# Kernel tuning notes

Measured on AMD Instinct MI355X. Metric: run time of the kernel, lower is better.

The kernel has to match this reference:

```python
import jax, jax.numpy as jnp
import numpy as np

DIM = 2048
Q_C = 1536
KV_C = 512
H = 16
DH = 128
DR = 64
EPS = 1e-6
B = 4
T = 2048


def rmsnorm(x, g, eps=EPS):
    var = jnp.mean(x * x, axis=-1, keepdims=True)
    return x * jax.lax.rsqrt(var + eps) * g


def apply_rope(x, freqs_cis):
    # x: [B, t, h, d]; freqs_cis: [t, d//2, 2] (cos, sin)
    xs = x.reshape(*x.shape[:-1], -1, 2)
    x1, x2 = xs[..., 0], xs[..., 1]
    cos = freqs_cis[None, :, None, :, 0]
    sin = freqs_cis[None, :, None, :, 1]
    o1 = x1 * cos - x2 * sin
    o2 = x1 * sin + x2 * cos
    return jnp.stack([o1, o2], axis=-1).reshape(x.shape)


def setup_inputs() -> dict:
    key = jax.random.key(0)
    ks = jax.random.split(key, 12)
    s = lambda fan_in: 1.0 / np.sqrt(fan_in)
    inp = {}
    inp["x"] = jax.random.normal(ks[0], (B, T, DIM), dtype=jnp.float32)
    inp["start_pos"] = 0
    # rotary frequencies for decoupled dim
    inv_freq = 1.0 / (10000.0 ** (np.arange(0, DR, 2, dtype=np.float32) / DR))
    angles = np.arange(T, dtype=np.float32)[:, None] * inv_freq[None, :]  # [T, DR//2]
    inp["freqs_cis"] = jnp.asarray(np.stack([np.cos(angles), np.sin(angles)], axis=-1))
    # causal additive mask
    neg = jnp.float32(-1e9)
    inp["mask"] = jnp.where(jnp.tril(jnp.ones((T, T), dtype=bool)), 0.0, neg).astype(jnp.float32)
    # weights stored as (in, out)
    inp["W_dq"] = jax.random.normal(ks[1], (DIM, Q_C), dtype=jnp.float32) * s(DIM)
    inp["W_uq"] = jax.random.normal(ks[2], (Q_C, H * DH), dtype=jnp.float32) * s(Q_C)
    inp["W_dkv"] = jax.random.normal(ks[3], (DIM, KV_C), dtype=jnp.float32) * s(DIM)
    inp["W_uk"] = jax.random.normal(ks[4], (KV_C, H * DH), dtype=jnp.float32) * s(KV_C)
    inp["W_uv"] = jax.random.normal(ks[5], (KV_C, H * DH), dtype=jnp.float32) * s(KV_C)
    inp["W_qr"] = jax.random.normal(ks[6], (Q_C, H * DR), dtype=jnp.float32) * s(Q_C)
    inp["W_kr"] = jax.random.normal(ks[7], (DIM, DR), dtype=jnp.float32) * s(DIM)
    inp["W_o"] = jax.random.normal(ks[8], (H * DH, DIM), dtype=jnp.float32) * s(H * DH)
    inp["g_q"] = jnp.ones((Q_C,), dtype=jnp.float32)
    inp["g_kv"] = jnp.ones((KV_C,), dtype=jnp.float32)
    return inp


def reference(x, start_pos, freqs_cis, mask, W_dq, W_uq, W_dkv, W_uk, W_uv, W_qr, W_kr, W_o, g_q, g_kv):
    Bc, t, _ = x.shape
    q_c = rmsnorm(x @ W_dq, g_q)            # [B, t, Q_C]
    kv_c = rmsnorm(x @ W_dkv, g_kv)         # [B, t, KV_C]
    q_rope = (q_c @ W_qr).reshape(Bc, t, H, DR)
    q_rope = apply_rope(q_rope, freqs_cis)
    k_rope = apply_rope((x @ W_kr)[:, :, None, :], freqs_cis)  # [B, t, 1, DR]
    k_rope = jnp.broadcast_to(k_rope, (Bc, t, H, DR))
    q = (q_c @ W_uq).reshape(Bc, t, H, DH)
    k = (kv_c @ W_uk).reshape(Bc, t, H, DH)
    v = (kv_c @ W_uv).reshape(Bc, t, H, DH)
    q = jnp.concatenate([q, q_rope], axis=-1)  # [B, t, H, DH+DR]
    k = jnp.concatenate([k, k_rope], axis=-1)
    scale = 1.0 / np.sqrt(DH + DR)
    scores = jnp.einsum("bqhd,bkhd->bhqk", q, k) * scale + mask
    probs = jax.nn.softmax(scores, axis=-1)
    out = jnp.einsum("bhqk,bkhd->bqhd", probs, v).reshape(Bc, t, H * DH)
    return out @ W_o
```

## Files before the change

### kernel.cpp

```cpp
#include <hip/hip_runtime.h>
#include <hip/hip_bf16.h>
#include <cstdint>
#include <cstddef>

typedef unsigned short u16;
typedef __attribute__((ext_vector_type(8))) short s8v;
typedef __attribute__((ext_vector_type(4))) float f4v;

__device__ __forceinline__ float bf2f(u16 u) {
  union { unsigned u; float f; } v; v.u = ((unsigned)u) << 16; return v.f;
}
__device__ __forceinline__ u16 f2bf(float f) {
  __hip_bfloat16 h = __float2bfloat16(f);
  return *reinterpret_cast<u16*>(&h);
}

__device__ __forceinline__ void async16(u16* lds, const u16* g) {
  __builtin_amdgcn_global_load_lds((const __attribute__((address_space(1))) void*)g,
                                   (__attribute__((address_space(3))) void*)lds,
                                   16, 0, 0);
}

__global__ __launch_bounds__(256) void k_f32_to_bf16(const float* __restrict__ in,
                                                     u16* __restrict__ out, int n8) {
  int i = blockIdx.x * 256 + threadIdx.x;
  if (i >= n8) return;
  const float4* p = (const float4*)(in + (size_t)i * 8);
  float4 a = p[0], b = p[1];
  s8v ov;
  ov[0] = (short)f2bf(a.x); ov[1] = (short)f2bf(a.y);
  ov[2] = (short)f2bf(a.z); ov[3] = (short)f2bf(a.w);
  ov[4] = (short)f2bf(b.x); ov[5] = (short)f2bf(b.y);
  ov[6] = (short)f2bf(b.z); ov[7] = (short)f2bf(b.w);
  *(s8v*)(out + (size_t)i * 8) = ov;
}

__global__ __launch_bounds__(256) void k_transpose_bf16(const float* __restrict__ W,
                                                        u16* __restrict__ Wt, int K, int N) {
  __shared__ float tile[32][33];
  int n0 = blockIdx.x * 32, k0 = blockIdx.y * 32;
  int tx = threadIdx.x & 31, ty = threadIdx.x >> 5;
#pragma unroll
  for (int i = 0; i < 32; i += 8)
    tile[ty + i][tx] = W[(size_t)(k0 + ty + i) * N + n0 + tx];
  __syncthreads();
#pragma unroll
  for (int i = 0; i < 32; i += 8)
    Wt[(size_t)(n0 + ty + i) * K + k0 + tx] = f2bf(tile[tx][ty + i]);
}

template <int BM, int BN, int WVM, int WVN, int EPI>
__global__ __launch_bounds__(256, 2) void k_gemm(const u16* __restrict__ A,
                                                 const u16* __restrict__ Bt,
                                                 void* __restrict__ C0v,
                                                 void* __restrict__ C1v,
                                                 int M, int N, int K, int split) {
  constexpr int FM = BM / WVM / 16, FN = BN / WVN / 16;
  __shared__ __align__(16) u16 As[BM * 32];
  __shared__ __align__(16) u16 Bs[BN * 32];
  const int tid = threadIdx.x, wv = tid >> 6, ln = tid & 63;
  const int lo = ln & 15, hi = ln >> 4;
  const int wr = wv / WVN, wc = wv % WVN;

  int nwg = gridDim.x, bid = blockIdx.x;
  int s = (bid & 7) * (nwg >> 3) + (bid >> 3);
  int gm = M / BM;
  int m0 = (s % gm) * BM, n0 = (s / gm) * BN;

  f4v acc[FM][FN] = {};

  for (int k0 = 0; k0 < K; k0 += 32) {
    __syncthreads();
#pragma unroll
    for (int i = 0; i < BM / 64; i++) {
      int r = i * 64 + wv * 16 + (ln >> 2);
      async16(&As[(i * 64 + wv * 16) * 32],
              A + (size_t)(m0 + r) * K + k0 + (ln & 3) * 8);
    }
#pragma unroll
    for (int i = 0; i < BN / 64; i++) {
      int r = i * 64 + wv * 16 + (ln >> 2);
      async16(&Bs[(i * 64 + wv * 16) * 32],
              Bt + (size_t)(n0 + r) * K + k0 + (ln & 3) * 8);
    }
    __syncthreads();

    s8v af[FM], bf[FN];
#pragma unroll
    for (int m = 0; m < FM; m++)
      af[m] = *(const s8v*)&As[(wr * FM * 16 + m * 16 + lo) * 32 + hi * 8];
#pragma unroll
    for (int n = 0; n < FN; n++)
      bf[n] = *(const s8v*)&Bs[(wc * FN * 16 + n * 16 + lo) * 32 + hi * 8];
#pragma unroll
    for (int m = 0; m < FM; m++)
#pragma unroll
      for (int n = 0; n < FN; n++)
        acc[m][n] = __builtin_amdgcn_mfma_f32_16x16x32_bf16(af[m], bf[n], acc[m][n], 0, 0, 0);
  }

  bool second = (n0 >= split);
#pragma unroll
  for (int m = 0; m < FM; m++)
#pragma unroll
    for (int n = 0; n < FN; n++)
#pragma unroll
      for (int j = 0; j < 4; j++) {
        int row = m0 + wr * FM * 16 + m * 16 + hi * 4 + j;
        int col = n0 + wc * FN * 16 + n * 16 + lo;
        float v = acc[m][n][j];
        if constexpr (EPI == 0) {
          ((u16*)C0v)[(size_t)row * N + col] = f2bf(v);
        } else if constexpr (EPI == 1) {
          ((float*)C0v)[(size_t)row * N + col] = v;
        } else if constexpr (EPI == 2) {
          if (second) ((u16*)C1v)[(size_t)row * 512 + (col - 1536)] = f2bf(v);
          else        ((u16*)C0v)[(size_t)row * 1536 + col] = f2bf(v);
        } else if constexpr (EPI == 3) {
          if (second) ((u16*)C1v)[(size_t)row * 1024 + (col - 2048)] = f2bf(v);
          else        ((u16*)C0v)[(size_t)row * 3072 + (col >> 7) * 192 + (col & 127)] = f2bf(v);
        } else {
          if (second) ((u16*)C1v)[(size_t)row * 2048 + (col - 2048)] = f2bf(v);
          else        ((u16*)C0v)[(size_t)row * 3072 + (col >> 7) * 192 + (col & 127)] = f2bf(v);
        }
      }
}

__global__ void k_rmsnorm(u16* __restrict__ buf, const float* __restrict__ g, int C) {
  int row = blockIdx.x;
  u16* p = buf + (size_t)row * C;
  int tid = threadIdx.x;
  float x[8];
  float ss = 0.f;
  s8v v = *(const s8v*)(p + tid * 8);
#pragma unroll
  for (int i = 0; i < 8; i++) { float xi = bf2f((u16)v[i]); x[i] = xi; ss += xi * xi; }
#pragma unroll
  for (int off = 1; off < 64; off <<= 1) ss += __shfl_xor(ss, off);
  __shared__ float red[4];
  if (tid < 4) red[tid] = 0.f;
  __syncthreads();
  if ((tid & 63) == 0) red[tid >> 6] = ss;
  __syncthreads();
  float sc = rsqrtf((red[0] + red[1] + red[2] + red[3]) / (float)C + 1e-6f);
  s8v ov;
#pragma unroll
  for (int i = 0; i < 8; i++) ov[i] = (short)f2bf(x[i] * sc * g[tid * 8 + i]);
  *(s8v*)(p + tid * 8) = ov;
}

__global__ __launch_bounds__(256) void k_rope_q(const u16* __restrict__ qr,
                                                const float* __restrict__ freqs,
                                                u16* __restrict__ qbuf) {
  int idx = blockIdx.x * 256 + threadIdx.x;
  int r = idx >> 4, h = idx & 15;
  int t = r & 2047;
  const u16* src = qr + (size_t)r * 1024 + h * 64;
  u16* dst = qbuf + (size_t)r * 3072 + h * 192 + 128;
  const float* fc = freqs + (size_t)t * 64;
  u16 in[64], out[64];
#pragma unroll
  for (int c = 0; c < 8; c++) {
    s8v vv = *(const s8v*)(src + c * 8);
#pragma unroll
    for (int e = 0; e < 8; e++) in[c * 8 + e] = (u16)vv[e];
  }
#pragma unroll
  for (int i = 0; i < 32; i++) {
    float x1 = bf2f(in[2 * i]), x2 = bf2f(in[2 * i + 1]);
    float co = fc[2 * i], si = fc[2 * i + 1];
    out[2 * i] = f2bf(x1 * co - x2 * si);
    out[2 * i + 1] = f2bf(x1 * si + x2 * co);
  }
#pragma unroll
  for (int c = 0; c < 8; c++) {
    s8v ov;
#pragma unroll
    for (int e = 0; e < 8; e++) ov[e] = (short)out[c * 8 + e];
    *(s8v*)(dst + c * 8) = ov;
  }
}

__global__ __launch_bounds__(256) void k_rope_k(const u16* __restrict__ kr,
                                                const float* __restrict__ freqs,
                                                u16* __restrict__ kbuf) {
  int idx = blockIdx.x * 256 + threadIdx.x;
  int r = idx >> 4, h = idx & 15;
  int t = r & 2047;
  const u16* src = kr + (size_t)r * 64;
  u16* dst = kbuf + (size_t)r * 3072 + h * 192 + 128;
  const float* fc = freqs + (size_t)t * 64;
  u16 in[64], out[64];
#pragma unroll
  for (int c = 0; c < 8; c++) {
    s8v vv = *(const s8v*)(src + c * 8);
#pragma unroll
    for (int e = 0; e < 8; e++) in[c * 8 + e] = (u16)vv[e];
  }
#pragma unroll
  for (int i = 0; i < 32; i++) {
    float x1 = bf2f(in[2 * i]), x2 = bf2f(in[2 * i + 1]);
    float co = fc[2 * i], si = fc[2 * i + 1];
    out[2 * i] = f2bf(x1 * co - x2 * si);
    out[2 * i + 1] = f2bf(x1 * si + x2 * co);
  }
#pragma unroll
  for (int c = 0; c < 8; c++) {
    s8v ov;
#pragma unroll
    for (int e = 0; e < 8; e++) ov[e] = (short)out[c * 8 + e];
    *(s8v*)(dst + c * 8) = ov;
  }
}

__global__ __launch_bounds__(256) void k_transpose_v(const u16* __restrict__ vtmp,
                                                     u16* __restrict__ vt) {
  __shared__ __align__(16) u16 tile[64][72];
  int r0 = blockIdx.x * 64, c0 = blockIdx.y * 64;
  int b = r0 >> 11, t0 = r0 & 2047;
  int h = c0 >> 7, d0 = c0 & 127;
  int tid = threadIdx.x;
  int ci = (tid & 7) * 8, ri = tid >> 3;
#pragma unroll
  for (int i = 0; i < 2; i++)
    *(s8v*)&tile[ri + 32 * i][ci] =
        *(const s8v*)(vtmp + (size_t)(r0 + ri + 32 * i) * 2048 + c0 + ci);
  __syncthreads();
  int tx = tid & 7, rr = tid >> 3;
#pragma unroll
  for (int i = 0; i < 2; i++) {
    int dr = rr + 32 * i;
    s8v ov;
#pragma unroll
    for (int e = 0; e < 8; e++) ov[e] = (short)tile[tx * 8 + e][dr];
    *(s8v*)(vt + (size_t)((b * 16 + h) * 128 + d0 + dr) * 2048 + t0 + tx * 8) = ov;
  }
}

__global__ __launch_bounds__(256, 3) void k_attn(const u16* __restrict__ Q,
                                                 const u16* __restrict__ K,
                                                 const u16* __restrict__ V,
                                                 u16* __restrict__ O) {
  __shared__ __align__(16) u16 Ks[64 * 192];
  __shared__ __align__(16) u16 Vs[128 * 64];
  __shared__ __align__(16) u16 p_lds[4][16 * 88];
  int bid = blockIdx.x;
  int lw = (bid & 7) * 256 + (bid >> 3);
  int qt = 31 - (lw & 31), h = (lw >> 5) & 15, b = lw >> 9;
  int tid = threadIdx.x, wv = tid >> 6, ln = tid & 63;
  int lo = ln & 15, hi = ln >> 4, lo7 = lo & 7;
  int qb = qt * 64 + wv * 16;

  const u16* qptr = Q + (size_t)(b * 2048 + qb + lo) * 3072 + h * 192 + hi * 8;
  s8v qf[6];
#pragma unroll
  for (int ks = 0; ks < 6; ks++) qf[ks] = *(const s8v*)(qptr + ks * 32);

  f4v Oa[8] = {};
  float m_r[4], lpart[4];
#pragma unroll
  for (int j = 0; j < 4; j++) { m_r[j] = -3e38f; lpart[j] = 0.f; }
  const float sl2 = 0.07216878364870323f * 1.44269504f;
  const float THRU = 11.5f / sl2;

  const u16* kg = K + (size_t)(b * 2048) * 3072 + h * 192;
  const u16* vg = V + (size_t)((b * 16 + h) * 128) * 2048;
  int kgo[6], klo[6];
#pragma unroll
  for (int i = 0; i < 6; i++) {
    int id = i * 256 + tid, r = id / 24, c = id % 24;
    kgo[i] = r * 3072 + c * 8;
    klo[i] = r * 192 + (c ^ (r & 7)) * 8;
  }
  int vgo[4], vlo[4];
#pragma unroll
  for (int i = 0; i < 4; i++) {
    int id = i * 256 + tid, r = id >> 3, c = id & 7;
    vgo[i] = r * 2048 + c * 8;
    vlo[i] = r * 64 + (c ^ (r & 7)) * 8;
  }

  u16* pl = p_lds[wv];
  int last = (qb + 15) >> 6;
  s8v kreg[6], vreg[4];

#pragma unroll
  for (int i = 0; i < 6; i++) kreg[i] = *(const s8v*)(kg + kgo[i]);
#pragma unroll
  for (int i = 0; i < 4; i++) vreg[i] = *(const s8v*)(vg + vgo[i]);
#pragma unroll
  for (int i = 0; i < 6; i++) *(s8v*)&Ks[klo[i]] = kreg[i];
#pragma unroll
  for (int i = 0; i < 4; i++) *(s8v*)&Vs[vlo[i]] = vreg[i];
  __syncthreads();

  for (int t = 0; t <= last; t++) {
    int kv0 = t * 64;
    if (t < last) {
      size_t ksh = (size_t)(kv0 + 64) * 3072;
#pragma unroll
      for (int i = 0; i < 6; i++) kreg[i] = *(const s8v*)(kg + ksh + kgo[i]);
#pragma unroll
      for (int i = 0; i < 4; i++) vreg[i] = *(const s8v*)(vg + (kv0 + 64) + vgo[i]);
    }

    f4v S[4] = {};
    __builtin_amdgcn_s_setprio(1);
#pragma unroll
    for (int ks = 0; ks < 6; ks++)
#pragma unroll
      for (int nf = 0; nf < 4; nf++) {
        s8v kf = *(const s8v*)&Ks[(nf * 16 + lo) * 192 + (((ks * 4 + hi) ^ lo7) * 8)];
        S[nf] = __builtin_amdgcn_mfma_f32_16x16x32_bf16(qf[ks], kf, S[nf], 0, 0, 0);
      }
    __builtin_amdgcn_s_setprio(0);

    float p[4][4], tmax[4];
#pragma unroll
    for (int j = 0; j < 4; j++) tmax[j] = -3e38f;
    if (t == last) {
#pragma unroll
      for (int nf = 0; nf < 4; nf++)
#pragma unroll
        for (int j = 0; j < 4; j++) {
          float sv = S[nf][j];
          if (kv0 + nf * 16 + lo > qb + hi * 4 + j) sv = -3e38f;
          p[nf][j] = sv;
          tmax[j] = fmaxf(tmax[j], sv);
        }
    } else {
#pragma unroll
      for (int nf = 0; nf < 4; nf++)
#pragma unroll
        for (int j = 0; j < 4; j++) {
          p[nf][j] = S[nf][j];
          tmax[j] = fmaxf(tmax[j], S[nf][j]);
        }
    }
    bool need = false;
#pragma unroll
    for (int j = 0; j < 4; j++) need = need || (tmax[j] > m_r[j] + THRU);
    if (__any(need)) {
#pragma unroll
      for (int off = 1; off < 16; off <<= 1)
#pragma unroll
        for (int j = 0; j < 4; j++) tmax[j] = fmaxf(tmax[j], __shfl_xor(tmax[j], off));
#pragma unroll
      for (int j = 0; j < 4; j++) {
        float nm = fmaxf(m_r[j], tmax[j]);
        float fj = exp2f((m_r[j] - nm) * sl2);
        m_r[j] = nm;
        lpart[j] *= fj;
#pragma unroll
        for (int df = 0; df < 8; df++) Oa[df][j] *= fj;
      }
    }
#pragma unroll
    for (int nf = 0; nf < 4; nf++)
#pragma unroll
      for (int j = 0; j < 4; j++) {
        float pv = exp2f((p[nf][j] - m_r[j]) * sl2);
        p[nf][j] = pv;
        lpart[j] += pv;
      }

#pragma unroll
    for (int nf = 0; nf < 4; nf++)
#pragma unroll
      for (int j = 0; j < 4; j++)
        pl[(hi * 4 + j) * 88 + nf * 16 + lo] = f2bf(p[nf][j]);

    __builtin_amdgcn_s_setprio(1);
#pragma unroll
    for (int ks2 = 0; ks2 < 2; ks2++) {
      s8v pa = *(const s8v*)&pl[lo * 88 + ks2 * 32 + hi * 8];
#pragma unroll
      for (int df = 0; df < 8; df++) {
        s8v vf = *(const s8v*)&Vs[(df * 16 + lo) * 64 + (((ks2 * 4 + hi) ^ lo7) * 8)];
        Oa[df] = __builtin_amdgcn_mfma_f32_16x16x32_bf16(pa, vf, Oa[df], 0, 0, 0);
      }
    }
    __builtin_amdgcn_s_setprio(0);

    __syncthreads();
    if (t < last) {
#pragma unroll
      for (int i = 0; i < 6; i++) *(s8v*)&Ks[klo[i]] = kreg[i];
#pragma unroll
      for (int i = 0; i < 4; i++) *(s8v*)&Vs[vlo[i]] = vreg[i];
      __syncthreads();
    }
  }

#pragma unroll
  for (int off = 1; off < 16; off <<= 1)
#pragma unroll
    for (int j = 0; j < 4; j++) lpart[j] += __shfl_xor(lpart[j], off);

#pragma unroll
  for (int j = 0; j < 4; j++) {
    float inv = 1.0f / lpart[j];
    u16* orow = O + (size_t)(b * 2048 + qb + hi * 4 + j) * 2048 + h * 128;
#pragma unroll
    for (int df = 0; df < 8; df++) orow[df * 16 + lo] = f2bf(Oa[df][j] * inv);
  }
}

extern "C" void kernel_launch(void* const* d_in, const int* in_sizes, int n_in,
                              void* d_out, int out_size, void* d_ws, size_t ws_size,
                              hipStream_t stream) {
  (void)in_sizes; (void)n_in; (void)out_size; (void)ws_size;
  const float* x     = (const float*)d_in[0];
  const float* freqs = (const float*)d_in[2];
  const float* W_dq  = (const float*)d_in[4];
  const float* W_uq  = (const float*)d_in[5];
  const float* W_dkv = (const float*)d_in[6];
  const float* W_uk  = (const float*)d_in[7];
  const float* W_uv  = (const float*)d_in[8];
  const float* W_qr  = (const float*)d_in[9];
  const float* W_kr  = (const float*)d_in[10];
  const float* W_o   = (const float*)d_in[11];
  const float* g_q   = (const float*)d_in[12];
  const float* g_kv  = (const float*)d_in[13];
  float* out = (float*)d_out;

  const int M = 8192;
  char* w = (char*)d_ws;
  auto alloc = [&](size_t n) { char* p = w; w += (n + 255) & ~(size_t)255; return p; };

  u16* xb     = (u16*)alloc((size_t)M * 2048 * 2);
  u16* wdq    = (u16*)alloc((size_t)1536 * 2048 * 2);
  u16* wdkv   = (u16*)alloc((size_t)512 * 2048 * 2);
  u16* wuq    = (u16*)alloc((size_t)2048 * 1536 * 2);
  u16* wqr    = (u16*)alloc((size_t)1024 * 1536 * 2);
  u16* wuk    = (u16*)alloc((size_t)2048 * 512 * 2);
  u16* wuv    = (u16*)alloc((size_t)2048 * 512 * 2);
  u16* wkr    = (u16*)alloc((size_t)64 * 2048 * 2);
  u16* wo     = (u16*)alloc((size_t)2048 * 2048 * 2);
  u16* q_c    = (u16*)alloc((size_t)M * 1536 * 2);
  u16* kv_c   = (u16*)alloc((size_t)M * 512 * 2);
  u16* qr_raw = (u16*)alloc((size_t)M * 1024 * 2);
  u16* kr_raw = (u16*)alloc((size_t)M * 64 * 2);
  u16* qbuf   = (u16*)alloc((size_t)M * 3072 * 2);
  u16* kbuf   = (u16*)alloc((size_t)M * 3072 * 2);
  u16* vt     = (u16*)alloc((size_t)M * 2048 * 2);
  u16* vtmp = xb;
  u16* aout = xb;

  k_f32_to_bf16<<<M * 2048 / 8 / 256, 256, 0, stream>>>(x, xb, M * 2048 / 8);
  k_transpose_bf16<<<dim3(1536 / 32, 2048 / 32), 256, 0, stream>>>(W_dq, wdq, 2048, 1536);
  k_transpose_bf16<<<dim3(512 / 32, 2048 / 32), 256, 0, stream>>>(W_dkv, wdkv, 2048, 512);
  k_transpose_bf16<<<dim3(2048 / 32, 1536 / 32), 256, 0, stream>>>(W_uq, wuq, 1536, 2048);
  k_transpose_bf16<<<dim3(1024 / 32, 1536 / 32), 256, 0, stream>>>(W_qr, wqr, 1536, 1024);
  k_transpose_bf16<<<dim3(2048 / 32, 512 / 32), 256, 0, stream>>>(W_uk, wuk, 512, 2048);
  k_transpose_bf16<<<dim3(2048 / 32, 512 / 32), 256, 0, stream>>>(W_uv, wuv, 512, 2048);
  k_transpose_bf16<<<dim3(64 / 32, 2048 / 32), 256, 0, stream>>>(W_kr, wkr, 2048, 64);
  k_transpose_bf16<<<dim3(2048 / 32, 2048 / 32), 256, 0, stream>>>(W_o, wo, 2048, 2048);

  k_gemm<128, 128, 2, 2, 2><<<(M / 128) * (2048 / 128), 256, 0, stream>>>(
      xb, wdq, q_c, kv_c, M, 2048, 2048, 1536);
  k_rmsnorm<<<M, 192, 0, stream>>>(q_c, g_q, 1536);
  k_rmsnorm<<<M, 64, 0, stream>>>(kv_c, g_kv, 512);

  k_gemm<128, 128, 2, 2, 3><<<(M / 128) * (3072 / 128), 256, 0, stream>>>(
      q_c, wuq, qbuf, qr_raw, M, 3072, 1536, 2048);
  k_rope_q<<<M * 16 / 256, 256, 0, stream>>>(qr_raw, freqs, qbuf);

  k_gemm<128, 64, 4, 1, 0><<<(M / 128) * (64 / 64), 256, 0, stream>>>(
      xb, wkr, kr_raw, nullptr, M, 64, 2048, 1 << 30);
  k_rope_k<<<M * 16 / 256, 256, 0, stream>>>(kr_raw, freqs, kbuf);

  k_gemm<128, 128, 2, 2, 4><<<(M / 128) * (4096 / 128), 256, 0, stream>>>(
      kv_c, wuk, kbuf, vtmp, M, 4096, 512, 2048);
  k_transpose_v<<<dim3(M / 64, 2048 / 64), 256, 0, stream>>>(vtmp, vt);

  k_attn<<<4 * 16 * 32, 256, 0, stream>>>(qbuf, kbuf, vt, aout);

  k_gemm<128, 128, 2, 2, 1><<<(M / 128) * (2048 / 128), 256, 0, stream>>>(
      aout, wo, out, nullptr, M, 2048, 2048, 1 << 30);
}
```

Baseline: 855.2 us.

## Replace GEMMs with 256x256 8-wave pipelined kernel and merge weight transposes

Replaces the simple 128x128 four-wave GEMM with a 256x256 tile, 512-thread kernel. It uses 128KB of XOR-swizzled LDS, double buffering, and interleaved async loads with MFMA phases gated by vmcnt waits and barriers. This raises data reuse per tile and overlaps memory traffic with compute. The eight weight-transpose launches are merged into one, the small K-rope projection gets its own kernel, and setprio hints are removed from attention. The risks are lower occupancy from the large LDS use and fewer workgroups on the small GEMMs.

```diff
diff --git a/kernel.cpp b/kernel.cpp
--- a/kernel.cpp
+++ b/kernel.cpp
@@ -35,10 +35,23 @@
   *(s8v*)(out + (size_t)i * 8) = ov;
 }
 
-__global__ __launch_bounds__(256) void k_transpose_bf16(const float* __restrict__ W,
-                                                        u16* __restrict__ Wt, int K, int N) {
+__global__ __launch_bounds__(256) void k_transpose_all(
+    const float* w0, const float* w1, const float* w2, const float* w3,
+    const float* w4, const float* w5, const float* w6, const float* w7,
+    u16* t0, u16* t1, u16* t2, u16* t3, u16* t4, u16* t5, u16* t6, u16* t7) {
+  int bid = blockIdx.x;
+  const float* W; u16* Wt; int K, N, lb;
+  if (bid < 3072)       { W = w0; Wt = t0; K = 2048; N = 1536; lb = bid; }
+  else if (bid < 4096)  { W = w1; Wt = t1; K = 2048; N = 512;  lb = bid - 3072; }
+  else if (bid < 7168)  { W = w2; Wt = t2; K = 1536; N = 2048; lb = bid - 4096; }
+  else if (bid < 8704)  { W = w3; Wt = t3; K = 1536; N = 1024; lb = bid - 7168; }
+  else if (bid < 9728)  { W = w4; Wt = t4; K = 512;  N = 2048; lb = bid - 8704; }
+  else if (bid < 10752) { W = w5; Wt = t5; K = 512;  N = 2048; lb = bid - 9728; }
+  else if (bid < 10880) { W = w6; Wt = t6; K = 2048; N = 64;   lb = bid - 10752; }
+  else                  { W = w7; Wt = t7; K = 2048; N = 2048; lb = bid - 10880; }
+  int nb = N >> 5;
+  int n0 = (lb % nb) * 32, k0 = (lb / nb) * 32;
   __shared__ float tile[32][33];
-  int n0 = blockIdx.x * 32, k0 = blockIdx.y * 32;
   int tx = threadIdx.x & 31, ty = threadIdx.x >> 5;
 #pragma unroll
   for (int i = 0; i < 32; i += 8)
@@ -49,69 +62,138 @@
     Wt[(size_t)(n0 + ty + i) * K + k0 + tx] = f2bf(tile[tx][ty + i]);
 }
 
-template <int BM, int BN, int WVM, int WVN, int EPI>
-__global__ __launch_bounds__(256, 2) void k_gemm(const u16* __restrict__ A,
-                                                 const u16* __restrict__ Bt,
-                                                 void* __restrict__ C0v,
-                                                 void* __restrict__ C1v,
-                                                 int M, int N, int K, int split) {
-  constexpr int FM = BM / WVM / 16, FN = BN / WVN / 16;
-  __shared__ __align__(16) u16 As[BM * 32];
-  __shared__ __align__(16) u16 Bs[BN * 32];
+template <int EPI>
+__global__ __launch_bounds__(512, 2) void k_gemm8(const u16* __restrict__ A,
+                                                  const u16* __restrict__ Bt,
+                                                  void* __restrict__ C0v,
+                                                  void* __restrict__ C1v,
+                                                  int M, int N, int K, int split) {
+  __shared__ __align__(16) u16 lds[65536];
   const int tid = threadIdx.x, wv = tid >> 6, ln = tid & 63;
   const int lo = ln & 15, hi = ln >> 4;
-  const int wr = wv / WVN, wc = wv % WVN;
+  const int wm = wv >> 2, wn = wv & 3;
 
   int nwg = gridDim.x, bid = blockIdx.x;
   int s = (bid & 7) * (nwg >> 3) + (bid >> 3);
-  int gm = M / BM;
-  int m0 = (s % gm) * BM, n0 = (s / gm) * BN;
-
-  f4v acc[FM][FN] = {};
-
-  for (int k0 = 0; k0 < K; k0 += 32) {
-    __syncthreads();
-#pragma unroll
-    for (int i = 0; i < BM / 64; i++) {
-      int r = i * 64 + wv * 16 + (ln >> 2);
-      async16(&As[(i * 64 + wv * 16) * 32],
-              A + (size_t)(m0 + r) * K + k0 + (ln & 3) * 8);
-    }
-#pragma unroll
-    for (int i = 0; i < BN / 64; i++) {
-      int r = i * 64 + wv * 16 + (ln >> 2);
-      async16(&Bs[(i * 64 + wv * 16) * 32],
-              Bt + (size_t)(n0 + r) * K + k0 + (ln & 3) * 8);
-    }
-    __syncthreads();
-
-    s8v af[FM], bf[FN];
-#pragma unroll
-    for (int m = 0; m < FM; m++)
-      af[m] = *(const s8v*)&As[(wr * FM * 16 + m * 16 + lo) * 32 + hi * 8];
-#pragma unroll
-    for (int n = 0; n < FN; n++)
-      bf[n] = *(const s8v*)&Bs[(wc * FN * 16 + n * 16 + lo) * 32 + hi * 8];
-#pragma unroll
-    for (int m = 0; m < FM; m++)
-#pragma unroll
-      for (int n = 0; n < FN; n++)
-        acc[m][n] = __builtin_amdgcn_mfma_f32_16x16x32_bf16(af[m], bf[n], acc[m][n], 0, 0, 0);
+  int gm = M >> 8;
+  int m0 = (s % gm) << 8, n0 = (s / gm) << 8;
+  int nt = K >> 6;
+
+  const int r8 = ln >> 3, c8 = ln & 7;
+  const int swz = (c8 ^ r8) * 8;
+  const u16* pa[2]; const u16* pb[2];
+#pragma unroll
+  for (int i = 0; i < 2; i++) {
+    pa[i] = A + (size_t)(m0 + i * 64 + wv * 8 + r8) * K + swz;
+    pb[i] = Bt + (size_t)(n0 + i * 64 + wv * 8 + r8) * K + swz;
+  }
+  const int sb0 = wv * 512, sb1 = 4096 + wv * 512;
+
+  auto stage = [&](int mat, int h, int kt2) {
+    int reg = (((kt2 & 1) * 2 + mat) * 2 + h) * 8192;
+    const u16* g0 = (mat ? pb[0] : pa[0]) + (size_t)h * 128 * K + kt2 * 64;
+    const u16* g1 = (mat ? pb[1] : pa[1]) + (size_t)h * 128 * K + kt2 * 64;
+    async16(&lds[reg + sb0], g0);
+    async16(&lds[reg + sb1], g1);
+  };
+
+  const int axor = lo & 7;
+  const int cc0 = (hi ^ axor) * 8;
+  const int cc1 = ((4 + hi) ^ axor) * 8;
+  const u16* aB = &lds[wm * 8192 + lo * 64];
+  const u16* bB = &lds[16384 + (wn >> 1) * 8192 + ((wn & 1) * 64 + lo) * 64];
+
+  f4v acc[8][4] = {};
+
+  stage(1, 0, 0); stage(1, 1, 0); stage(0, 0, 0); stage(0, 1, 0);
+  stage(1, 0, 1); stage(1, 1, 1); stage(0, 0, 1);
+  asm volatile("s_waitcnt vmcnt(6)" ::: "memory");
+  __builtin_amdgcn_s_barrier();
+
+  for (int kt = 0; kt < nt; ++kt) {
+    const int db32 = (kt & 1) * 32768;
+    s8v af[4][2], bf[4][2];
+#pragma unroll
+    for (int mi = 0; mi < 4; mi++) {
+      af[mi][0] = *(const s8v*)(aB + db32 + mi * 1024 + cc0);
+      af[mi][1] = *(const s8v*)(aB + db32 + mi * 1024 + cc1);
+    }
+#pragma unroll
+    for (int ni = 0; ni < 4; ni++) {
+      bf[ni][0] = *(const s8v*)(bB + db32 + ni * 1024 + cc0);
+      bf[ni][1] = *(const s8v*)(bB + db32 + ni * 1024 + cc1);
+    }
+    if (kt + 1 < nt) stage(0, 1, kt + 1);
+    __builtin_amdgcn_s_barrier();
+    __builtin_amdgcn_s_setprio(1);
+#pragma unroll
+    for (int mi = 0; mi < 4; mi++)
+#pragma unroll
+      for (int ni = 0; ni < 2; ni++)
+#pragma unroll
+        for (int kk = 0; kk < 2; kk++)
+          acc[mi][ni] = __builtin_amdgcn_mfma_f32_16x16x32_bf16(af[mi][kk], bf[ni][kk], acc[mi][ni], 0, 0, 0);
+    __builtin_amdgcn_s_setprio(0);
+    __builtin_amdgcn_s_barrier();
+    if (kt + 2 < nt) stage(1, 0, kt + 2);
+    __builtin_amdgcn_s_barrier();
+    __builtin_amdgcn_s_setprio(1);
+#pragma unroll
+    for (int mi = 0; mi < 4; mi++)
+#pragma unroll
+      for (int ni = 2; ni < 4; ni++)
+#pragma unroll
+        for (int kk = 0; kk < 2; kk++)
+          acc[mi][ni] = __builtin_amdgcn_mfma_f32_16x16x32_bf16(af[mi][kk], bf[ni][kk], acc[mi][ni], 0, 0, 0);
+    __builtin_amdgcn_s_setprio(0);
+    __builtin_amdgcn_s_barrier();
+#pragma unroll
+    for (int mi = 0; mi < 4; mi++) {
+      af[mi][0] = *(const s8v*)(aB + db32 + (mi + 4) * 1024 + cc0);
+      af[mi][1] = *(const s8v*)(aB + db32 + (mi + 4) * 1024 + cc1);
+    }
+    if (kt + 2 < nt) stage(1, 1, kt + 2);
+    __builtin_amdgcn_s_barrier();
+    __builtin_amdgcn_s_setprio(1);
+#pragma unroll
+    for (int mi = 0; mi < 4; mi++)
+#pragma unroll
+      for (int ni = 2; ni < 4; ni++)
+#pragma unroll
+        for (int kk = 0; kk < 2; kk++)
+          acc[mi + 4][ni] = __builtin_amdgcn_mfma_f32_16x16x32_bf16(af[mi][kk], bf[ni][kk], acc[mi + 4][ni], 0, 0, 0);
+    __builtin_amdgcn_s_setprio(0);
+    __builtin_amdgcn_s_barrier();
+    if (kt + 2 < nt) {
+      stage(0, 0, kt + 2);
+      asm volatile("s_waitcnt vmcnt(6)" ::: "memory");
+    } else {
+      asm volatile("s_waitcnt vmcnt(0)" ::: "memory");
+    }
+    __builtin_amdgcn_s_barrier();
+    __builtin_amdgcn_s_setprio(1);
+#pragma unroll
+    for (int mi = 0; mi < 4; mi++)
+#pragma unroll
+      for (int ni = 0; ni < 2; ni++)
+#pragma unroll
+        for (int kk = 0; kk < 2; kk++)
+          acc[mi + 4][ni] = __builtin_amdgcn_mfma_f32_16x16x32_bf16(af[mi][kk], bf[ni][kk], acc[mi + 4][ni], 0, 0, 0);
+    __builtin_amdgcn_s_setprio(0);
+    __builtin_amdgcn_s_barrier();
   }
 
   bool second = (n0 >= split);
 #pragma unroll
-  for (int m = 0; m < FM; m++)
-#pragma unroll
-    for (int n = 0; n < FN; n++)
+  for (int mi = 0; mi < 8; mi++)
+#pragma unroll
+    for (int ni = 0; ni < 4; ni++)
 #pragma unroll
       for (int j = 0; j < 4; j++) {
-        int row = m0 + wr * FM * 16 + m * 16 + hi * 4 + j;
-        int col = n0 + wc * FN * 16 + n * 16 + lo;
-        float v = acc[m][n][j];
-        if constexpr (EPI == 0) {
-          ((u16*)C0v)[(size_t)row * N + col] = f2bf(v);
-        } else if constexpr (EPI == 1) {
+        int row = m0 + wm * 128 + mi * 16 + hi * 4 + j;
+        int col = n0 + wn * 64 + ni * 16 + lo;
+        float v = acc[mi][ni][j];
+        if constexpr (EPI == 1) {
           ((float*)C0v)[(size_t)row * N + col] = v;
         } else if constexpr (EPI == 2) {
           if (second) ((u16*)C1v)[(size_t)row * 512 + (col - 1536)] = f2bf(v);
@@ -123,6 +205,57 @@
           if (second) ((u16*)C1v)[(size_t)row * 2048 + (col - 2048)] = f2bf(v);
           else        ((u16*)C0v)[(size_t)row * 3072 + (col >> 7) * 192 + (col & 127)] = f2bf(v);
         }
+      }
+}
+
+__global__ __launch_bounds__(256, 2) void k_gemm_kr(const u16* __restrict__ A,
+                                                    const u16* __restrict__ Bt,
+                                                    u16* __restrict__ C,
+                                                    int M, int N, int K) {
+  constexpr int BM = 128, BN = 64, FM = 2, FN = 4;
+  __shared__ __align__(16) u16 As[BM * 32];
+  __shared__ __align__(16) u16 Bs[BN * 32];
+  const int tid = threadIdx.x, wv = tid >> 6, ln = tid & 63;
+  const int lo = ln & 15, hi = ln >> 4;
+  int nwg = gridDim.x, bid = blockIdx.x;
+  int sblk = (bid & 7) * (nwg >> 3) + (bid >> 3);
+  int gm = M / BM;
+  int m0 = (sblk % gm) * BM, n0 = (sblk / gm) * BN;
+  f4v acc[FM][FN] = {};
+  for (int k0 = 0; k0 < K; k0 += 32) {
+    __syncthreads();
+#pragma unroll
+    for (int i = 0; i < BM / 64; i++) {
+      int r = i * 64 + wv * 16 + (ln >> 2);
+      async16(&As[(i * 64 + wv * 16) * 32], A + (size_t)(m0 + r) * K + k0 + (ln & 3) * 8);
+    }
+    {
+      int r = wv * 16 + (ln >> 2);
+      async16(&Bs[(wv * 16) * 32], Bt + (size_t)(n0 + r) * K + k0 + (ln & 3) * 8);
+    }
+    __syncthreads();
+    s8v af[FM], bf[FN];
+#pragma unroll
+    for (int m = 0; m < FM; m++)
+      af[m] = *(const s8v*)&As[(wv * FM * 16 + m * 16 + lo) * 32 + hi * 8];
+#pragma unroll
+    for (int n = 0; n < FN; n++)
+      bf[n] = *(const s8v*)&Bs[(n * 16 + lo) * 32 + hi * 8];
+#pragma unroll
+    for (int m = 0; m < FM; m++)
+#pragma unroll
+      for (int n = 0; n < FN; n++)
+        acc[m][n] = __builtin_amdgcn_mfma_f32_16x16x32_bf16(af[m], bf[n], acc[m][n], 0, 0, 0);
+  }
+#pragma unroll
+  for (int m = 0; m < FM; m++)
+#pragma unroll
+    for (int n = 0; n < FN; n++)
+#pragma unroll
+      for (int j = 0; j < 4; j++) {
+        int row = m0 + wv * FM * 16 + m * 16 + hi * 4 + j;
+        int col = n0 + n * 16 + lo;
+        C[(size_t)row * N + col] = f2bf(acc[m][n][j]);
       }
 }
 
@@ -305,7 +438,6 @@
     }
 
     f4v S[4] = {};
-    __builtin_amdgcn_s_setprio(1);
 #pragma unroll
     for (int ks = 0; ks < 6; ks++)
 #pragma unroll
@@ -313,7 +445,6 @@
         s8v kf = *(const s8v*)&Ks[(nf * 16 + lo) * 192 + (((ks * 4 + hi) ^ lo7) * 8)];
         S[nf] = __builtin_amdgcn_mfma_f32_16x16x32_bf16(qf[ks], kf, S[nf], 0, 0, 0);
       }
-    __builtin_amdgcn_s_setprio(0);
 
     float p[4][4], tmax[4];
 #pragma unroll
@@ -370,7 +501,6 @@
       for (int j = 0; j < 4; j++)
         pl[(hi * 4 + j) * 88 + nf * 16 + lo] = f2bf(p[nf][j]);
 
-    __builtin_amdgcn_s_setprio(1);
 #pragma unroll
     for (int ks2 = 0; ks2 < 2; ks2++) {
       s8v pa = *(const s8v*)&pl[lo * 88 + ks2 * 32 + hi * 8];
@@ -380,7 +510,6 @@
         Oa[df] = __builtin_amdgcn_mfma_f32_16x16x32_bf16(pa, vf, Oa[df], 0, 0, 0);
       }
     }
-    __builtin_amdgcn_s_setprio(0);
 
     __syncthreads();
     if (t < last) {
@@ -448,34 +577,27 @@
   u16* aout = xb;
 
   k_f32_to_bf16<<<M * 2048 / 8 / 256, 256, 0, stream>>>(x, xb, M * 2048 / 8);
-  k_transpose_bf16<<<dim3(1536 / 32, 2048 / 32), 256, 0, stream>>>(W_dq, wdq, 2048, 1536);
-  k_transpose_bf16<<<dim3(512 / 32, 2048 / 32), 256, 0, stream>>>(W_dkv, wdkv, 2048, 512);
-  k_transpose_bf16<<<dim3(2048 / 32, 1536 / 32), 256, 0, stream>>>(W_uq, wuq, 1536, 2048);
-  k_transpose_bf16<<<dim3(1024 / 32, 1536 / 32), 256, 0, stream>>>(W_qr, wqr, 1536, 1024);
-  k_transpose_bf16<<<dim3(2048 / 32, 512 / 32), 256, 0, stream>>>(W_uk, wuk, 512, 2048);
-  k_transpose_bf16<<<dim3(2048 / 32, 512 / 32), 256, 0, stream>>>(W_uv, wuv, 512, 2048);
-  k_transpose_bf16<<<dim3(64 / 32, 2048 / 32), 256, 0, stream>>>(W_kr, wkr, 2048, 64);
-  k_transpose_bf16<<<dim3(2048 / 32, 2048 / 32), 256, 0, stream>>>(W_o, wo, 2048, 2048);
-
-  k_gemm<128, 128, 2, 2, 2><<<(M / 128) * (2048 / 128), 256, 0, stream>>>(
+  k_transpose_all<<<14976, 256, 0, stream>>>(W_dq, W_dkv, W_uq, W_qr, W_uk, W_uv, W_kr, W_o,
+                                             wdq, wdkv, wuq, wqr, wuk, wuv, wkr, wo);
+
+  k_gemm8<2><<<(M / 256) * (2048 / 256), 512, 0, stream>>>(
       xb, wdq, q_c, kv_c, M, 2048, 2048, 1536);
   k_rmsnorm<<<M, 192, 0, stream>>>(q_c, g_q, 1536);
   k_rmsnorm<<<M, 64, 0, stream>>>(kv_c, g_kv, 512);
 
-  k_gemm<128, 128, 2, 2, 3><<<(M / 128) * (3072 / 128), 256, 0, stream>>>(
+  k_gemm8<3><<<(M / 256) * (3072 / 256), 512, 0, stream>>>(
       q_c, wuq, qbuf, qr_raw, M, 3072, 1536, 2048);
   k_rope_q<<<M * 16 / 256, 256, 0, stream>>>(qr_raw, freqs, qbuf);
 
-  k_gemm<128, 64, 4, 1, 0><<<(M / 128) * (64 / 64), 256, 0, stream>>>(
-      xb, wkr, kr_raw, nullptr, M, 64, 2048, 1 << 30);
+  k_gemm_kr<<<(M / 128) * (64 / 64), 256, 0, stream>>>(xb, wkr, kr_raw, M, 64, 2048);
   k_rope_k<<<M * 16 / 256, 256, 0, stream>>>(kr_raw, freqs, kbuf);
 
-  k_gemm<128, 128, 2, 2, 4><<<(M / 128) * (4096 / 128), 256, 0, stream>>>(
+  k_gemm8<4><<<(M / 256) * (4096 / 256), 512, 0, stream>>>(
       kv_c, wuk, kbuf, vtmp, M, 4096, 512, 2048);
   k_transpose_v<<<dim3(M / 64, 2048 / 64), 256, 0, stream>>>(vtmp, vt);
 
   k_attn<<<4 * 16 * 32, 256, 0, stream>>>(qbuf, kbuf, vt, aout);
 
-  k_gemm<128, 128, 2, 2, 1><<<(M / 128) * (2048 / 128), 256, 0, stream>>>(
+  k_gemm8<1><<<(M / 256) * (2048 / 256), 512, 0, stream>>>(
       aout, wo, out, nullptr, M, 2048, 2048, 1 << 30);
 }
```

After: 791.2 us. -7.5%, faster.
